# Performance work log

Measured on AMD Instinct MI355X. Metric: run time of the kernel, lower is better.

The kernel has to match this reference:

```python
import jax, jax.numpy as jnp
import numpy as np

def setup_inputs() -> dict:
    key = jax.random.key(0)
    k1, k2, k3 = jax.random.split(key, 3)
    N_net, d, n_t, n_in = 1, 4, 2048, 256
    n_h, n = 8, 256
    STD = 0.02  # E_std / Q_std in the original init
    r_prime = jax.random.normal(k1, (N_net, d, n_t, n_in), dtype=jnp.float32)
    Q = STD * jax.random.normal(k2, (N_net, n_h, n_in, n_in), dtype=jnp.float32)
    E = STD * jax.random.normal(k3, (N_net, n_h, n, n_in), dtype=jnp.float32)
    return {"r_prime": r_prime, "Q": Q, "E": E}

def reference(r_prime, Q, E):
    # r_prime: [N, b, t, i_in]; Q: [N, h, i_in, j_in]; E: [N, h, n, j_in]
    n_t = r_prime.shape[2]
    # Omega[N,b,h,t,u] = r_t^T Q^h r_u  (bilinear attention scores, no softmax)
    Omega = jnp.einsum('Nbti,Nhij,Nbuj->Nbhtu', r_prime, Q, r_prime)
    # Causal mask (lower-triangular Theta), applied inside the second contraction.
    Theta = jnp.tril(jnp.ones((n_t, n_t), dtype=r_prime.dtype))
    # r[N,b,t,i_out] = sum_{u<=t,h} Omega[t,u] * (E^h r_u)_i
    r = jnp.einsum('Nbhtu,tu,Nhij,Nbuj->Nbti', Omega, Theta, E, r_prime)
    return r
```

## Files before the change

### kernel.cpp

```cpp
#include <hip/hip_runtime.h>

typedef __attribute__((ext_vector_type(4))) float f32x4;
typedef __attribute__((ext_vector_type(8))) short s16x8;

#define DEVI static __device__ __forceinline__

constexpr int BB = 4, HH = 8, TT = 2048, DD = 256;

DEVI short f2bf(float f) {
  union { float f; unsigned u; } x; x.f = f;
  unsigned r = x.u + 0x7fffu + ((x.u >> 16) & 1u);
  return (short)(r >> 16);
}

DEVI void gl16(const short* g, short* l) {
  __builtin_amdgcn_global_load_lds(
      (const __attribute__((address_space(1))) void*)g,
      (__attribute__((address_space(3))) void*)l, 16, 0, 0);
}

__device__ const signed char g_jtt[24] = {15,15, 7,14,14,13,13, 6,12,12,11,11, 5,10,10, 9, 9, 4, 8, 8, 3, 2, 1, 0};
__device__ const signed char g_jlo[24] = { 0,32, 0, 0,30, 0,28, 0, 0,26, 0,24, 0, 0,22, 0,20, 0, 0,18, 0, 0, 0, 0};
__device__ const signed char g_jn [24] = {32,32,32,30,30,28,28,28,26,26,24,24,24,22,22,20,20,20,18,18,16,12, 8, 4};

__global__ void cast_rE(const float* __restrict__ r, const float* __restrict__ E,
                        short* __restrict__ rbf, short* __restrict__ Ebf) {
  int idx = blockIdx.x * blockDim.x + threadIdx.x;
  int stride = gridDim.x * blockDim.x;
  int nR = BB * TT * DD / 8, nE = HH * DD * DD / 8;
  for (int i = idx; i < nR; i += stride) {
    f32x4 x0 = ((const f32x4*)r)[2 * i], x1 = ((const f32x4*)r)[2 * i + 1];
    s16x8 o;
    #pragma unroll
    for (int e = 0; e < 4; ++e) { o[e] = f2bf(x0[e]); o[4 + e] = f2bf(x1[e]); }
    ((s16x8*)rbf)[i] = o;
  }
  for (int i = idx; i < nE; i += stride) {
    f32x4 x0 = ((const f32x4*)E)[2 * i], x1 = ((const f32x4*)E)[2 * i + 1];
    s16x8 o;
    #pragma unroll
    for (int e = 0; e < 4; ++e) { o[e] = f2bf(x0[e]); o[4 + e] = f2bf(x1[e]); }
    ((s16x8*)Ebf)[i] = o;
  }
}

__global__ void qt_prep(const float* __restrict__ Q, short* __restrict__ Qt) {
  __shared__ float t[64][65];
  int tid = threadIdx.x;
  int h = blockIdx.y, bx = blockIdx.x;
  int i0 = (bx >> 2) * 64, j0 = (bx & 3) * 64;
  const float* Qh = Q + (size_t)h * DD * DD;
  int rr = tid >> 2, cq = tid & 3;
  #pragma unroll
  for (int it = 0; it < 4; ++it) {
    int col = cq * 16 + it * 4;
    f32x4 v = *(const f32x4*)(Qh + (size_t)(i0 + rr) * DD + j0 + col);
    #pragma unroll
    for (int e = 0; e < 4; ++e) t[rr][col + e] = v[e];
  }
  __syncthreads();
  int j = tid >> 2, iq = tid & 3;
  short* dst = Qt + (size_t)h * DD * DD + (size_t)(j0 + j) * DD + i0;
  #pragma unroll
  for (int it = 0; it < 4; ++it) {
    int ic = iq * 16 + it * 4;
    short o[4];
    #pragma unroll
    for (int e = 0; e < 4; ++e) o[e] = f2bf(t[ic + e][j]);
    *(int2*)(dst + ic) = *(int2*)o;
  }
}

__global__ __launch_bounds__(256, 2)
void prep_gemm(const short* __restrict__ rbf, const short* __restrict__ Qt,
               const short* __restrict__ Ebf, short* __restrict__ Abf,
               short* __restrict__ Vtbf) {
  __shared__ __align__(16) short w_lds[64 * 256];
  int tid = threadIdx.x, lane = tid & 63, wid = tid >> 6;
  int h = blockIdx.y, b = blockIdx.z;
  int mode = blockIdx.x >> 7, bx = blockIdx.x & 127;
  const short* X; const short* W; short* C; int ldC, m0, n0;
  if (mode == 0) {
    m0 = (bx >> 2) * 64; n0 = (bx & 3) * 64;
    X = rbf + (size_t)b * TT * DD;
    W = Qt + (size_t)h * DD * DD;
    C = Abf + (size_t)(b * HH + h) * TT * DD; ldC = DD;
  } else {
    m0 = (bx & 3) * 64; n0 = (bx >> 2) * 64;
    X = Ebf + (size_t)h * DD * DD;
    W = rbf + (size_t)b * TT * DD;
    C = Vtbf + (size_t)(b * HH + h) * DD * TT; ldC = TT;
  }
  #pragma unroll
  for (int it = 0; it < 8; ++it) {
    int t = it * 256 + tid;
    int row = t >> 5, kb = t & 31;
    s16x8 v = *(const s16x8*)(W + (size_t)(n0 + row) * DD + kb * 8);
    *(s16x8*)(&w_lds[row * 256 + ((kb ^ (row & 7)) << 3)]) = v;
  }
  s16x8 a[8];
  {
    const short* xrow = X + (size_t)(m0 + wid * 16 + (lane & 15)) * DD + (lane >> 4) * 8;
    #pragma unroll
    for (int ks = 0; ks < 8; ++ks) a[ks] = *(const s16x8*)(xrow + ks * 32);
  }
  __syncthreads();
  f32x4 c[4] = {};
  #pragma unroll
  for (int n = 0; n < 4; ++n) {
    int row = n * 16 + (lane & 15);
    #pragma unroll
    for (int ks = 0; ks < 8; ++ks) {
      int kb = ks * 4 + (lane >> 4);
      s16x8 bfr = *(const s16x8*)(&w_lds[row * 256 + ((kb ^ (row & 7)) << 3)]);
      c[n] = __builtin_amdgcn_mfma_f32_16x16x32_bf16(a[ks], bfr, c[n], 0, 0, 0);
    }
  }
  __syncthreads();
  #pragma unroll
  for (int n = 0; n < 4; ++n) {
    int col = n * 16 + (lane & 15);
    int cb = col >> 3;
    #pragma unroll
    for (int rr = 0; rr < 4; ++rr) {
      int row = wid * 16 + (lane >> 4) * 4 + rr;
      w_lds[row * 64 + ((cb ^ (row & 7)) << 3) + (col & 7)] = f2bf(c[n][rr]);
    }
  }
  __syncthreads();
  #pragma unroll
  for (int q = 0; q < 2; ++q) {
    int t = q * 256 + tid;
    int row = t >> 3, cb = t & 7;
    s16x8 v = *(const s16x8*)(&w_lds[row * 64 + ((cb ^ (row & 7)) << 3)]);
    *(s16x8*)(&C[(size_t)(m0 + row) * ldC + n0 + cb * 8]) = v;
  }
}

__global__ __launch_bounds__(256, 2)
void attn_main(const short* __restrict__ Abf, const short* __restrict__ Kbf,
               const short* __restrict__ Vtb, float* __restrict__ out) {
  __shared__ __align__(16) short k_lds[2][32 * 256];
  __shared__ __align__(16) short v_lds[2][256 * 32];
  __shared__ __align__(16) short s_lds[128 * 32];
  int tid = threadIdx.x, lane = tid & 63, wid = tid >> 6;
  int q = blockIdx.x;
  int jj = q >> 5, hb = q & 31;
  int h = hb >> 2, b = hb & 3;
  int tt = g_jtt[jj];
  int u_lo = g_jlo[jj];
  int u_n = g_jn[jj];

  const short* Ab0 = Abf + (size_t)(b * HH + h) * TT * DD;
  const short* Kb = Kbf + (size_t)b * TT * DD;
  const short* Vb = Vtb + (size_t)(b * HH + h) * DD * TT;

#define STAGE(bufi, iu_) do {                                                  \
    int U_ = (iu_) * 32;                                                       \
    _Pragma("unroll")                                                          \
    for (int c_ = 0; c_ < 4; ++c_) {           \
      int kc_ = wid * 4 + c_;                                                  \
      int row_ = kc_ * 2 + (lane >> 5);                                        \
      int blk_ = lane & 31;                                                    \
      gl16(Kb + (size_t)(U_ + row_) * DD + ((blk_ ^ (row_ & 7)) << 3),         \
           &k_lds[bufi][kc_ * 512]);                                           \
    }                                                                          \
    _Pragma("unroll")                                                          \
    for (int c_ = 0; c_ < 4; ++c_) {           \
      int vc_ = wid * 4 + c_;                                                  \
      int row_ = vc_ * 16 + (lane >> 2);                                       \
      int blk_ = lane & 3;                                                     \
      gl16(Vb + (size_t)row_ * TT + U_ + ((blk_ ^ ((row_ >> 1) & 3)) << 3),    \
           &v_lds[bufi][vc_ * 512]);                                           \
    }                                                                          \
  } while (0)

  s16x8 a[2][8];
  {
    const short* abase = Ab0 + (size_t)(tt * 128 + wid * 32 + (lane & 15)) * DD + ((lane >> 4) << 3);
    #pragma unroll
    for (int rb = 0; rb < 2; ++rb)
      #pragma unroll
      for (int ks = 0; ks < 8; ++ks)
        a[rb][ks] = *(const s16x8*)(abase + rb * 16 * DD + ks * 32);
  }
  f32x4 acc[2][16] = {};

  STAGE(0, u_lo);

  #pragma unroll 1
  for (int s2 = 0; s2 < u_n; ++s2) {
    int cur = s2 & 1;
    asm volatile("s_waitcnt vmcnt(0)" ::: "memory");
    asm volatile("s_waitcnt lgkmcnt(0)" ::: "memory");
    __builtin_amdgcn_s_barrier();
    if (s2 + 1 < u_n) STAGE(cur ^ 1, u_lo + s2 + 1);
    __builtin_amdgcn_s_setprio(1);
    int U = (u_lo + s2) * 32;

    f32x4 s[2][2] = {{{0,0,0,0},{0,0,0,0}},{{0,0,0,0},{0,0,0,0}}};
    #pragma unroll
    for (int n2 = 0; n2 < 2; ++n2) {
      int row = n2 * 16 + (lane & 15);
      #pragma unroll
      for (int ks = 0; ks < 8; ++ks) {
        int kb = ks * 4 + (lane >> 4);
        s16x8 bfr = *(const s16x8*)(&k_lds[cur][row * 256 + ((kb ^ (row & 7)) << 3)]);
        s[0][n2] = __builtin_amdgcn_mfma_f32_16x16x32_bf16(a[0][ks], bfr, s[0][n2], 0, 0, 0);
        s[1][n2] = __builtin_amdgcn_mfma_f32_16x16x32_bf16(a[1][ks], bfr, s[1][n2], 0, 0, 0);
      }
    }
    #pragma unroll
    for (int rb = 0; rb < 2; ++rb) {
      #pragma unroll
      for (int n2 = 0; n2 < 2; ++n2) {
        #pragma unroll
        for (int rr = 0; rr < 4; ++rr) {
          int t_loc = wid * 32 + rb * 16 + (lane >> 4) * 4 + rr;
          int u_glob = U + n2 * 16 + (lane & 15);
          float v = (u_glob <= tt * 128 + t_loc) ? s[rb][n2][rr] : 0.0f;
          int kloc = n2 * 16 + (lane & 15);
          int cb = kloc >> 3;
          s_lds[t_loc * 32 + ((cb ^ ((t_loc >> 1) & 3)) << 3) + (kloc & 7)] = f2bf(v);
        }
      }
    }
    s16x8 af[2];
    #pragma unroll
    for (int rb = 0; rb < 2; ++rb) {
      int R = wid * 32 + rb * 16 + (lane & 15);
      int cb2 = (lane >> 4) ^ ((R >> 1) & 3);
      af[rb] = *(const s16x8*)(&s_lds[R * 32 + (cb2 << 3)]);
    }
    #pragma unroll
    for (int ni = 0; ni < 16; ++ni) {
      int vrow = ni * 16 + (lane & 15);
      int ub = (lane >> 4) ^ ((vrow >> 1) & 3);
      s16x8 bv = *(const s16x8*)(&v_lds[cur][vrow * 32 + (ub << 3)]);
      acc[0][ni] = __builtin_amdgcn_mfma_f32_16x16x32_bf16(af[0], bv, acc[0][ni], 0, 0, 0);
      acc[1][ni] = __builtin_amdgcn_mfma_f32_16x16x32_bf16(af[1], bv, acc[1][ni], 0, 0, 0);
    }
    __builtin_amdgcn_s_setprio(0);
  }

  float* ob = out + ((size_t)b * TT + tt * 128 + wid * 32) * DD;
  #pragma unroll
  for (int rb = 0; rb < 2; ++rb) {
    #pragma unroll
    for (int ni = 0; ni < 16; ++ni) {
      int col = ni * 16 + (lane & 15);
      #pragma unroll
      for (int rr = 0; rr < 4; ++rr) {
        int row = rb * 16 + (lane >> 4) * 4 + rr;
        atomicAdd(&ob[row * DD + col], acc[rb][ni][rr]);
      }
    }
  }
#undef STAGE
}

extern "C" void kernel_launch(void* const* d_in, const int* in_sizes, int n_in,
                              void* d_out, int out_size, void* d_ws, size_t ws_size,
                              hipStream_t stream) {
  const float* r = (const float*)d_in[0];
  const float* Q = (const float*)d_in[1];
  const float* E = (const float*)d_in[2];
  float* out = (float*)d_out;
  char* ws = (char*)d_ws;

  size_t off = 0;
  short* rbf = (short*)(ws + off); off += (size_t)BB * TT * DD * 2;
  short* Qt  = (short*)(ws + off); off += (size_t)HH * DD * DD * 2;
  short* Ebf = (short*)(ws + off); off += (size_t)HH * DD * DD * 2;
  short* Abf = (short*)(ws + off); off += (size_t)BB * HH * TT * DD * 2;
  short* Vtb = (short*)(ws + off); off += (size_t)BB * HH * DD * TT * 2;

  hipMemsetAsync(d_out, 0, (size_t)out_size * sizeof(float), stream);
  cast_rE<<<1024, 256, 0, stream>>>(r, E, rbf, Ebf);
  qt_prep<<<dim3(16, HH), 256, 0, stream>>>(Q, Qt);
  prep_gemm<<<dim3(256, HH, BB), 256, 0, stream>>>(rbf, Qt, Ebf, Abf, Vtb);
  attn_main<<<dim3(768, 1, 1), 256, 0, stream>>>(Abf, rbf, Vtb, out);
}
```

Baseline: 239.4 us.

## Deepen attention K/V prefetch to two stages and interleave block scheduling

The attention kernel now keeps two K/V tiles in flight instead of one. It waits with a partial vmcnt so the next stage's loads stay outstanding, and adds an end-of-iteration barrier before refilling the buffer just consumed. Async LDS loads are issued through inline asm that sets m0, using one dynamic shared buffer. Block indices are remapped so consecutive blocks share head and batch across different tile-rows, which is meant to improve L2 reuse and balance the triangular work. The aim is to hide global-load latency better, at the cost of an extra barrier per iteration and more fragile hand-written waitcnt logic.

```diff
diff --git a/kernel.cpp b/kernel.cpp
--- a/kernel.cpp
+++ b/kernel.cpp
@@ -11,12 +11,6 @@
   union { float f; unsigned u; } x; x.f = f;
   unsigned r = x.u + 0x7fffu + ((x.u >> 16) & 1u);
   return (short)(r >> 16);
-}
-
-DEVI void gl16(const short* g, short* l) {
-  __builtin_amdgcn_global_load_lds(
-      (const __attribute__((address_space(1))) void*)g,
-      (__attribute__((address_space(3))) void*)l, 16, 0, 0);
 }
 
 __device__ const signed char g_jtt[24] = {15,15, 7,14,14,13,13, 6,12,12,11,11, 5,10,10, 9, 9, 4, 8, 8, 3, 2, 1, 0};
@@ -140,12 +134,11 @@
 __global__ __launch_bounds__(256, 2)
 void attn_main(const short* __restrict__ Abf, const short* __restrict__ Kbf,
                const short* __restrict__ Vtb, float* __restrict__ out) {
-  __shared__ __align__(16) short k_lds[2][32 * 256];
-  __shared__ __align__(16) short v_lds[2][256 * 32];
-  __shared__ __align__(16) short s_lds[128 * 32];
+  extern __shared__ __align__(16) char smem[];
   int tid = threadIdx.x, lane = tid & 63, wid = tid >> 6;
   int q = blockIdx.x;
-  int jj = q >> 5, hb = q & 31;
+  int jj = (q & 7) | ((q >> 8) << 3);
+  int hb = (q >> 3) & 31;
   int h = hb >> 2, b = hb & 3;
   int tt = g_jtt[jj];
   int u_lo = g_jlo[jj];
@@ -155,23 +148,29 @@
   const short* Kb = Kbf + (size_t)b * TT * DD;
   const short* Vb = Vtb + (size_t)(b * HH + h) * DD * TT;
 
-#define STAGE(bufi, iu_) do {                                                  \
+#define STAGE(bufsel, iu_) do {                                                \
     int U_ = (iu_) * 32;                                                       \
     _Pragma("unroll")                                                          \
     for (int c_ = 0; c_ < 4; ++c_) {           \
       int kc_ = wid * 4 + c_;                                                  \
       int row_ = kc_ * 2 + (lane >> 5);                                        \
       int blk_ = lane & 31;                                                    \
-      gl16(Kb + (size_t)(U_ + row_) * DD + ((blk_ ^ (row_ & 7)) << 3),         \
-           &k_lds[bufi][kc_ * 512]);                                           \
+      const short* gp_ = Kb + (size_t)(U_ + row_) * DD + ((blk_ ^ (row_ & 7)) << 3); \
+      int lo_ = __builtin_amdgcn_readfirstlane((bufsel) * 16384 + kc_ * 1024); \
+      asm volatile("s_mov_b32 m0, %1\n\t"                                      \
+                   "global_load_lds_dwordx4 %0, off"                           \
+                   :: "v"(gp_), "s"(lo_) : "memory");                          \
     }                                                                          \
     _Pragma("unroll")                                                          \
     for (int c_ = 0; c_ < 4; ++c_) {           \
       int vc_ = wid * 4 + c_;                                                  \
       int row_ = vc_ * 16 + (lane >> 2);                                       \
       int blk_ = lane & 3;                                                     \
-      gl16(Vb + (size_t)row_ * TT + U_ + ((blk_ ^ ((row_ >> 1) & 3)) << 3),    \
-           &v_lds[bufi][vc_ * 512]);                                           \
+      const short* gp_ = Vb + (size_t)row_ * TT + U_ + ((blk_ ^ ((row_ >> 1) & 3)) << 3); \
+      int lo_ = __builtin_amdgcn_readfirstlane(32768 + (bufsel) * 16384 + vc_ * 1024); \
+      asm volatile("s_mov_b32 m0, %1\n\t"                                      \
+                   "global_load_lds_dwordx4 %0, off"                           \
+                   :: "v"(gp_), "s"(lo_) : "memory");                          \
     }                                                                          \
   } while (0)
 
@@ -184,17 +183,31 @@
       for (int ks = 0; ks < 8; ++ks)
         a[rb][ks] = *(const s16x8*)(abase + rb * 16 * DD + ks * 32);
   }
+  #pragma unroll
+  for (int rb = 0; rb < 2; ++rb)
+    #pragma unroll
+    for (int ks = 0; ks < 8; ++ks)
+      asm volatile("" :: "v"(a[rb][ks]));
+
   f32x4 acc[2][16] = {};
 
   STAGE(0, u_lo);
+  STAGE(1, u_lo + 1);
+
+  short* sl = (short*)(smem + 65536);
 
   #pragma unroll 1
   for (int s2 = 0; s2 < u_n; ++s2) {
     int cur = s2 & 1;
-    asm volatile("s_waitcnt vmcnt(0)" ::: "memory");
-    asm volatile("s_waitcnt lgkmcnt(0)" ::: "memory");
+    if (s2 + 1 < u_n) {
+      asm volatile("s_waitcnt vmcnt(8)" ::: "memory");
+    } else {
+      asm volatile("s_waitcnt vmcnt(0)" ::: "memory");
+    }
+    __builtin_amdgcn_sched_barrier(0);
     __builtin_amdgcn_s_barrier();
-    if (s2 + 1 < u_n) STAGE(cur ^ 1, u_lo + s2 + 1);
+    const short* kl = (const short*)(smem + cur * 16384);
+    const short* vl = (const short*)(smem + 32768 + cur * 16384);
     __builtin_amdgcn_s_setprio(1);
     int U = (u_lo + s2) * 32;
 
@@ -205,7 +218,7 @@
       #pragma unroll
       for (int ks = 0; ks < 8; ++ks) {
         int kb = ks * 4 + (lane >> 4);
-        s16x8 bfr = *(const s16x8*)(&k_lds[cur][row * 256 + ((kb ^ (row & 7)) << 3)]);
+        s16x8 bfr = *(const s16x8*)(&kl[row * 256 + ((kb ^ (row & 7)) << 3)]);
         s[0][n2] = __builtin_amdgcn_mfma_f32_16x16x32_bf16(a[0][ks], bfr, s[0][n2], 0, 0, 0);
         s[1][n2] = __builtin_amdgcn_mfma_f32_16x16x32_bf16(a[1][ks], bfr, s[1][n2], 0, 0, 0);
       }
@@ -221,7 +234,7 @@
           float v = (u_glob <= tt * 128 + t_loc) ? s[rb][n2][rr] : 0.0f;
           int kloc = n2 * 16 + (lane & 15);
           int cb = kloc >> 3;
-          s_lds[t_loc * 32 + ((cb ^ ((t_loc >> 1) & 3)) << 3) + (kloc & 7)] = f2bf(v);
+          sl[t_loc * 32 + ((cb ^ ((t_loc >> 1) & 3)) << 3) + (kloc & 7)] = f2bf(v);
         }
       }
     }
@@ -230,17 +243,21 @@
     for (int rb = 0; rb < 2; ++rb) {
       int R = wid * 32 + rb * 16 + (lane & 15);
       int cb2 = (lane >> 4) ^ ((R >> 1) & 3);
-      af[rb] = *(const s16x8*)(&s_lds[R * 32 + (cb2 << 3)]);
+      af[rb] = *(const s16x8*)(&sl[R * 32 + (cb2 << 3)]);
     }
     #pragma unroll
     for (int ni = 0; ni < 16; ++ni) {
       int vrow = ni * 16 + (lane & 15);
       int ub = (lane >> 4) ^ ((vrow >> 1) & 3);
-      s16x8 bv = *(const s16x8*)(&v_lds[cur][vrow * 32 + (ub << 3)]);
+      s16x8 bv = *(const s16x8*)(&vl[vrow * 32 + (ub << 3)]);
       acc[0][ni] = __builtin_amdgcn_mfma_f32_16x16x32_bf16(af[0], bv, acc[0][ni], 0, 0, 0);
       acc[1][ni] = __builtin_amdgcn_mfma_f32_16x16x32_bf16(af[1], bv, acc[1][ni], 0, 0, 0);
     }
     __builtin_amdgcn_s_setprio(0);
+    asm volatile("s_waitcnt lgkmcnt(0)" ::: "memory");
+    __builtin_amdgcn_sched_barrier(0);
+    __builtin_amdgcn_s_barrier();
+    if (s2 + 2 < u_n) STAGE(cur, u_lo + s2 + 2);
   }
 
   float* ob = out + ((size_t)b * TT + tt * 128 + wid * 32) * DD;
@@ -279,5 +296,5 @@
   cast_rE<<<1024, 256, 0, stream>>>(r, E, rbf, Ebf);
   qt_prep<<<dim3(16, HH), 256, 0, stream>>>(Q, Qt);
   prep_gemm<<<dim3(256, HH, BB), 256, 0, stream>>>(rbf, Qt, Ebf, Abf, Vtb);
-  attn_main<<<dim3(768, 1, 1), 256, 0, stream>>>(Abf, rbf, Vtb, out);
-}
+  attn_main<<<dim3(768, 1, 1), 256, 73728, stream>>>(Abf, rbf, Vtb, out);
+}
```

Result: slower. 298.0 us (+24.5%).
